# Optimization experiments

Hardware: AMD Instinct MI355X
Metric: run time of the kernel (lower is better)

## Reference

```python
import jax, jax.numpy as jnp
import numpy as np

N_NODES = 100000
N_EDGES = 3200000
IN_DIM = 256
HID = 16
OUT = 10


def setup_inputs() -> dict:
    key = jax.random.key(0)
    k1, k2, k3, k4, k5, k6 = jax.random.split(key, 6)
    x = jax.random.normal(k1, (N_NODES, IN_DIM), dtype=jnp.float32)
    edge_index = jax.random.randint(k2, (2, N_EDGES), 0, N_NODES, dtype=jnp.int64)
    # Glorot-style init for GCN weights, zeros for bias (PyG defaults)
    W1 = jax.random.normal(k3, (IN_DIM, HID), dtype=jnp.float32) * (1.0 / np.sqrt(IN_DIM))
    b1 = jnp.zeros((HID,), dtype=jnp.float32)
    W2 = jax.random.normal(k4, (HID, OUT), dtype=jnp.float32) * (1.0 / np.sqrt(HID))
    b2 = jnp.zeros((OUT,), dtype=jnp.float32)
    return {"x": x, "edge_index": edge_index, "W1": W1, "b1": b1, "W2": W2, "b2": b2}


def _gcn_conv(h, src, dst, W, b, num_nodes):
    # GCNConv(normalize=False): out_i = sum_{(j->i) in E} (h_j W) + b
    m = h @ W                                   # [N, F_out] small GEMM
    agg = jax.ops.segment_sum(m[src], dst, num_segments=num_nodes)  # gather+scatter-add
    return agg + b


def reference(x, edge_index, W1, b1, W2, b2):
    src = edge_index[0]  # message source (flow: source_to_target)
    dst = edge_index[1]
    n = x.shape[0]
    h = jax.nn.relu(_gcn_conv(x, src, dst, W1, b1, n))
    # F.dropout with module in eval mode -> identity
    out = _gcn_conv(h, src, dst, W2, b2, n)
    return out
```

## Files before the change

kernel.cpp:

```cpp
#include <hip/hip_runtime.h>
#include <hip/hip_bf16.h>
#include <stdint.h>

#define IN_DIM 256
#define HID 16
#define OUTD 10
#define BKT_SHIFT 8
#define BKT_W 256
#define PART_CH 4096
#define EPT 16

typedef short v8s __attribute__((ext_vector_type(8)));
typedef float v4f __attribute__((ext_vector_type(4)));

__device__ __forceinline__ float bf2f(unsigned short u) {
    return __uint_as_float(((unsigned int)u) << 16);
}
__device__ __forceinline__ unsigned short f2bf(float f) {
    unsigned int u = __float_as_uint(f);
    unsigned int lsb = (u >> 16) & 1u;
    u += 0x7fffu + lsb;
    return (unsigned short)(u >> 16);
}

__device__ __forceinline__ int load_dst(const void* ei, int n_edges, int e, int is64) {
    return is64 ? (int)((const long long*)ei)[(size_t)n_edges + e]
                : ((const int*)ei)[(size_t)n_edges + e];
}
__device__ __forceinline__ int load_src(const void* ei, int n_edges, int e, int is64) {
    return is64 ? (int)((const long long*)ei)[e] : ((const int*)ei)[e];
}

__global__ void setup_kernel(const void* __restrict__ x,
                             const void* __restrict__ W1,
                             const void* __restrict__ ei,
                             int n_nodes, int* __restrict__ flags,
                             int* __restrict__ bucket_cnt, int K) {
    int t = threadIdx.x;
    for (int i = t; i < K; i += blockDim.x) bucket_cnt[i] = 0;
    if (t < 64) {
        const unsigned short* xs = (const unsigned short*)x;
        const unsigned short* ws = (const unsigned short*)W1;
        bool badx = false, badw = false;
#pragma unroll
        for (int q = 0; q < 4; ++q) {
            float vx = bf2f(xs[t + 64 * q]);
            float vw = bf2f(ws[t + 64 * q]);
            if (!(vx > -1e4f && vx < 1e4f)) badx = true;
            if (!(vw > -1e4f && vw < 1e4f)) badw = true;
        }
        const unsigned long long* e64 = (const unsigned long long*)ei;
        bool big = false;
#pragma unroll
        for (int q = 0; q < 2; ++q)
            if (e64[t + 64 * q] >= (unsigned long long)n_nodes) big = true;
        int xf32 = __any(badx) ? 1 : 0;
        int wf32 = __any(badw) ? 1 : 0;
        int is64 = __any(big) ? 0 : 1;
        if (t == 0) { flags[0] = is64; flags[1] = xf32; flags[2] = wf32; }
    }
}

__global__ void w1prep_kernel(const void* __restrict__ W1p,
                              unsigned short* __restrict__ W1split,
                              const int* __restrict__ flags) {
    const int wf32 = flags[2];
    int i = threadIdx.x + blockIdx.x * blockDim.x;
    if (i >= IN_DIM * HID) return;
    float w = wf32 ? ((const float*)W1p)[i]
                   : bf2f(((const unsigned short*)W1p)[i]);
    unsigned short hi = f2bf(w);
    unsigned short lo = f2bf(w - bf2f(hi));
    int k = i >> 4, n = i & 15;
    int kk = k >> 5, qd = (k >> 3) & 3, j = k & 7;
    int idx = ((kk * 4 + qd) * 16 + n) * 8 + j;
    W1split[idx] = hi;
    W1split[4096 + idx] = lo;
}

__global__ void bhist_kernel(const void* __restrict__ ei, int n_edges,
                             int* __restrict__ bucket_cnt,
                             const int* __restrict__ flags, int K) {
    extern __shared__ int lh[];
    for (int i = threadIdx.x; i < K; i += blockDim.x) lh[i] = 0;
    __syncthreads();
    int is64 = flags[0];
    int t = blockIdx.x * blockDim.x + threadIdx.x;
    int stride = gridDim.x * blockDim.x;
    for (int e = t; e < n_edges; e += stride) {
        int d = load_dst(ei, n_edges, e, is64);
        atomicAdd(&lh[d >> BKT_SHIFT], 1);
    }
    __syncthreads();
    for (int i = threadIdx.x; i < K; i += blockDim.x)
        if (lh[i]) atomicAdd(&bucket_cnt[i], lh[i]);
}

__global__ void bscan_kernel(const int* __restrict__ bucket_cnt, int K,
                             int* __restrict__ bucket_off, int* __restrict__ bcur,
                             int* __restrict__ row_off, int n_nodes, int n_edges) {
    __shared__ int ts[256];
    int t = threadIdx.x;
    const int KP = (K + 255) / 256;
    int base = t * KP;
    int local[8];
    int s = 0;
    for (int q = 0; q < KP; ++q) {
        int idx = base + q;
        int v = (idx < K) ? bucket_cnt[idx] : 0;
        local[q] = v; s += v;
    }
    ts[t] = s;
    __syncthreads();
    for (int off = 1; off < 256; off <<= 1) {
        int v = (t >= off) ? ts[t - off] : 0;
        __syncthreads();
        ts[t] += v;
        __syncthreads();
    }
    int ex = ts[t] - s;
    for (int q = 0; q < KP; ++q) {
        int idx = base + q;
        if (idx < K) { bucket_off[idx] = ex; bcur[idx] = ex; }
        ex += local[q];
    }
    if (t == 255) bucket_off[K] = ex;
    if (t == 0) row_off[n_nodes] = n_edges;
}

__global__ void part_kernel(const void* __restrict__ ei, int n_edges,
                            int* __restrict__ bcur, unsigned int* __restrict__ pairs,
                            const int* __restrict__ flags, int K) {
    __shared__ int lh[512];
    __shared__ int gdelta[512];
    __shared__ int ts[256];
    __shared__ unsigned int spairs[PART_CH];
    __shared__ unsigned short sbkt[PART_CH];
    int begin = blockIdx.x * PART_CH;
    int is64 = flags[0];
    int t = threadIdx.x;
    lh[t] = 0; lh[t + 256] = 0;

    int dloc[EPT];
#pragma unroll
    for (int i = 0; i < EPT; ++i) {
        int e = begin + i * 256 + t;
        dloc[i] = (e < n_edges) ? load_dst(ei, n_edges, e, is64) : -1;
    }
    __syncthreads();
#pragma unroll
    for (int i = 0; i < EPT; ++i)
        if (dloc[i] >= 0) atomicAdd(&lh[dloc[i] >> BKT_SHIFT], 1);
    __syncthreads();

    int c0 = lh[2 * t], c1 = lh[2 * t + 1];
    int s = c0 + c1;
    ts[t] = s;
    __syncthreads();
    for (int off = 1; off < 256; off <<= 1) {
        int v = (t >= off) ? ts[t - off] : 0;
        __syncthreads();
        ts[t] += v;
        __syncthreads();
    }
    int ex = ts[t] - s;
    if (c0 > 0) gdelta[2 * t]     = atomicAdd(&bcur[2 * t], c0) - ex;
    if (c1 > 0) gdelta[2 * t + 1] = atomicAdd(&bcur[2 * t + 1], c1) - (ex + c0);
    __syncthreads();
    lh[2 * t] = ex; lh[2 * t + 1] = ex + c0;
    __syncthreads();

#pragma unroll
    for (int i = 0; i < EPT; ++i) {
        int e = begin + i * 256 + t;
        if (dloc[i] >= 0) {
            int srcv = load_src(ei, n_edges, e, is64);
            int b = dloc[i] >> BKT_SHIFT;
            int lpos = atomicAdd(&lh[b], 1);
            spairs[lpos] = ((unsigned)srcv << 8) | ((unsigned)dloc[i] & (BKT_W - 1));
            sbkt[lpos] = (unsigned short)b;
        }
    }
    __syncthreads();

    int total = n_edges - begin; if (total > PART_CH) total = PART_CH;
    for (int j = t; j < total; j += 256)
        pairs[gdelta[sbkt[j]] + j] = spairs[j];
}

__global__ void csr_kernel(const unsigned int* __restrict__ pairs,
                           const int* __restrict__ bucket_off,
                           int* __restrict__ row_off, int* __restrict__ csr_src,
                           int n_nodes) {
    __shared__ int deg[BKT_W];
    __shared__ int cur[BKT_W];
    __shared__ int ts[BKT_W];
    int blk = blockIdx.x;
    int nbase = blk << BKT_SHIFT;
    int NL = n_nodes - nbase; if (NL > BKT_W) NL = BKT_W;
    int beg = bucket_off[blk], end = bucket_off[blk + 1];
    int t = threadIdx.x;
    if (t < BKT_W) deg[t] = 0;
    __syncthreads();
    for (int k = beg + t; k < end; k += blockDim.x)
        atomicAdd(&deg[pairs[k] & (BKT_W - 1)], 1);
    __syncthreads();
    if (t < BKT_W) ts[t] = deg[t];
    __syncthreads();
    for (int off = 1; off < BKT_W; off <<= 1) {
        int v = 0;
        if (t < BKT_W && t >= off) v = ts[t - off];
        __syncthreads();
        if (t < BKT_W) ts[t] += v;
        __syncthreads();
    }
    if (t < BKT_W) {
        int ex = beg + ts[t] - deg[t];
        cur[t] = ex;
        if (t < NL) row_off[nbase + t] = ex;
    }
    __syncthreads();
    for (int k = beg + t; k < end; k += blockDim.x) {
        unsigned int p = pairs[k];
        int pos = atomicAdd(&cur[p & (BKT_W - 1)], 1);
        csr_src[pos] = (int)(p >> 8);
    }
}

__global__ __launch_bounds__(256, 4) void gemm1_kernel(
        const void* __restrict__ xp_,
        const unsigned short* __restrict__ W1split,
        unsigned short* __restrict__ m1, int n_nodes,
        const int* __restrict__ flags) {
    const int xf32 = flags[1];
    int t = threadIdx.x;
    int lane = t & 63;
    int wave = t >> 6;
    int col  = lane & 15;
    int quad = lane >> 4;
    int n_tiles = (n_nodes + 15) >> 4;
    const unsigned short* Whi = W1split;
    const unsigned short* Wlo = W1split + 4096;

    if (!xf32) {
        const unsigned short* x = (const unsigned short*)xp_;
        for (int tile = blockIdx.x * 4 + wave; tile < n_tiles; tile += gridDim.x * 4) {
            int row = tile * 16 + col;
            int r = row < n_nodes ? row : n_nodes - 1;
            const unsigned short* xp = x + (size_t)r * IN_DIM + quad * 8;
            v8s a[8];
#pragma unroll
            for (int kk = 0; kk < 8; ++kk)
                a[kk] = *(const v8s*)(xp + kk * 32);
            v4f acc1 = {0.f, 0.f, 0.f, 0.f};
            v4f acc2 = {0.f, 0.f, 0.f, 0.f};
#pragma unroll
            for (int kk = 0; kk < 8; ++kk) {
                v8s bh = *(const v8s*)&Whi[(kk * 64 + lane) * 8];
                v8s bl = *(const v8s*)&Wlo[(kk * 64 + lane) * 8];
                acc1 = __builtin_amdgcn_mfma_f32_16x16x32_bf16(a[kk], bh, acc1, 0, 0, 0);
                acc2 = __builtin_amdgcn_mfma_f32_16x16x32_bf16(a[kk], bl, acc2, 0, 0, 0);
            }
#pragma unroll
            for (int rg = 0; rg < 4; ++rg) {
                int node = tile * 16 + quad * 4 + rg;
                if (node < n_nodes)
                    m1[(size_t)node * HID + col] = f2bf(acc1[rg] + acc2[rg]);
            }
        }
    } else {
        const float* x = (const float*)xp_;
        for (int tile = blockIdx.x * 4 + wave; tile < n_tiles; tile += gridDim.x * 4) {
            int row = tile * 16 + col;
            int r = row < n_nodes ? row : n_nodes - 1;
            const float* xp = x + (size_t)r * IN_DIM + quad * 8;
            float4 u[16];
#pragma unroll
            for (int kk = 0; kk < 8; ++kk) {
                u[2 * kk]     = *(const float4*)(xp + kk * 32);
                u[2 * kk + 1] = *(const float4*)(xp + kk * 32 + 4);
            }
            v4f acc1 = {0.f, 0.f, 0.f, 0.f};
            v4f acc2 = {0.f, 0.f, 0.f, 0.f};
#pragma unroll
            for (int kk = 0; kk < 8; ++kk) {
                float uv[8] = {u[2 * kk].x,     u[2 * kk].y,
                               u[2 * kk].z,     u[2 * kk].w,
                               u[2 * kk + 1].x, u[2 * kk + 1].y,
                               u[2 * kk + 1].z, u[2 * kk + 1].w};
                v8s ahi, alo;
#pragma unroll
                for (int j = 0; j < 8; ++j) {
                    unsigned short hi = f2bf(uv[j]);
                    unsigned short lo = f2bf(uv[j] - bf2f(hi));
                    ahi[j] = (short)hi; alo[j] = (short)lo;
                }
                v8s bh = *(const v8s*)&Whi[(kk * 64 + lane) * 8];
                v8s bl = *(const v8s*)&Wlo[(kk * 64 + lane) * 8];
                acc1 = __builtin_amdgcn_mfma_f32_16x16x32_bf16(ahi, bh, acc1, 0, 0, 0);
                acc2 = __builtin_amdgcn_mfma_f32_16x16x32_bf16(ahi, bl, acc2, 0, 0, 0);
                acc2 = __builtin_amdgcn_mfma_f32_16x16x32_bf16(alo, bh, acc2, 0, 0, 0);
            }
#pragma unroll
            for (int rg = 0; rg < 4; ++rg) {
                int node = tile * 16 + quad * 4 + rg;
                if (node < n_nodes)
                    m1[(size_t)node * HID + col] = f2bf(acc1[rg] + acc2[rg]);
            }
        }
    }
}

__device__ __forceinline__ v4f gather_bf16(const unsigned short* __restrict__ src,
                                           const int* __restrict__ csr_src,
                                           int beg, int end, int q) {
    float a0 = 0.f, a1 = 0.f, a2 = 0.f, a3 = 0.f;
    int k = beg;
    for (; k + 16 <= end; k += 16) {
        uint2 v[16];
#pragma unroll
        for (int u = 0; u < 16; ++u) {
            int s = csr_src[k + u];
            v[u] = *(const uint2*)(src + (size_t)s * HID + q * 4);
        }
#pragma unroll
        for (int u = 0; u < 16; ++u) {
            a0 += bf2f((unsigned short)(v[u].x));
            a1 += bf2f((unsigned short)(v[u].x >> 16));
            a2 += bf2f((unsigned short)(v[u].y));
            a3 += bf2f((unsigned short)(v[u].y >> 16));
        }
    }
    for (; k + 4 <= end; k += 4) {
        uint2 v[4];
#pragma unroll
        for (int u = 0; u < 4; ++u) {
            int s = csr_src[k + u];
            v[u] = *(const uint2*)(src + (size_t)s * HID + q * 4);
        }
#pragma unroll
        for (int u = 0; u < 4; ++u) {
            a0 += bf2f((unsigned short)(v[u].x));
            a1 += bf2f((unsigned short)(v[u].x >> 16));
            a2 += bf2f((unsigned short)(v[u].y));
            a3 += bf2f((unsigned short)(v[u].y >> 16));
        }
    }
    for (; k < end; ++k) {
        int s = csr_src[k];
        uint2 v = *(const uint2*)(src + (size_t)s * HID + q * 4);
        a0 += bf2f((unsigned short)(v.x));
        a1 += bf2f((unsigned short)(v.x >> 16));
        a2 += bf2f((unsigned short)(v.y));
        a3 += bf2f((unsigned short)(v.y >> 16));
    }
    v4f r = {a0, a1, a2, a3};
    return r;
}

__global__ void agg1_kernel(const unsigned short* __restrict__ m1,
                            const int* __restrict__ row_off,
                            const int* __restrict__ csr_src,
                            const void* __restrict__ b1p,
                            unsigned short* __restrict__ h, int n_nodes,
                            const int* __restrict__ flags) {
    int t = blockIdx.x * blockDim.x + threadIdx.x;
    int node = t >> 2;
    if (node >= n_nodes) return;
    int q = t & 3;
    const int wf32 = flags[2];
    v4f a = gather_bf16(m1, csr_src, row_off[node], row_off[node + 1], q);
    float b0, b1v, b2v, b3;
    if (wf32) {
        const float* b = (const float*)b1p + q * 4;
        b0 = b[0]; b1v = b[1]; b2v = b[2]; b3 = b[3];
    } else {
        const unsigned short* b = (const unsigned short*)b1p + q * 4;
        b0 = bf2f(b[0]); b1v = bf2f(b[1]); b2v = bf2f(b[2]); b3 = bf2f(b[3]);
    }
    float r0 = fmaxf(a[0] + b0, 0.f);
    float r1 = fmaxf(a[1] + b1v, 0.f);
    float r2 = fmaxf(a[2] + b2v, 0.f);
    float r3 = fmaxf(a[3] + b3, 0.f);
    uint2 packed;
    packed.x = (unsigned int)f2bf(r0) | ((unsigned int)f2bf(r1) << 16);
    packed.y = (unsigned int)f2bf(r2) | ((unsigned int)f2bf(r3) << 16);
    *(uint2*)(h + (size_t)node * HID + q * 4) = packed;
}

__global__ void agg2_out_kernel(const unsigned short* __restrict__ h,
                                const int* __restrict__ row_off,
                                const int* __restrict__ csr_src,
                                const void* __restrict__ W2p,
                                const void* __restrict__ b2p,
                                void* __restrict__ out, int n_nodes,
                                const int* __restrict__ flags) {
    __shared__ float Ws[HID * OUTD];
    __shared__ float bs[OUTD];
    const int xf32 = flags[1], wf32 = flags[2];
    if (threadIdx.x < HID * OUTD)
        Ws[threadIdx.x] = wf32 ? ((const float*)W2p)[threadIdx.x]
                               : bf2f(((const unsigned short*)W2p)[threadIdx.x]);
    if (threadIdx.x < OUTD)
        bs[threadIdx.x] = wf32 ? ((const float*)b2p)[threadIdx.x]
                               : bf2f(((const unsigned short*)b2p)[threadIdx.x]);
    __syncthreads();

    int t = blockIdx.x * blockDim.x + threadIdx.x;
    int node = t >> 2;
    if (node >= n_nodes) return;
    int q = t & 3;
    v4f a = gather_bf16(h, csr_src, row_off[node], row_off[node + 1], q);

    float o[OUTD];
#pragma unroll
    for (int od = 0; od < OUTD; ++od) {
        float s = 0.f;
#pragma unroll
        for (int j = 0; j < 4; ++j)
            s = fmaf(a[j], Ws[(q * 4 + j) * OUTD + od], s);
        o[od] = s;
    }
#pragma unroll
    for (int od = 0; od < OUTD; ++od) {
        o[od] += __shfl_xor(o[od], 1);
        o[od] += __shfl_xor(o[od], 2);
        o[od] += bs[od];
    }

    if (xf32) {
        float2* po = (float2*)((float*)out + (size_t)node * OUTD);
        if (q == 0) {
            po[0] = make_float2(o[0], o[1]);
            po[1] = make_float2(o[2], o[3]);
        } else if (q == 1) {
            po[2] = make_float2(o[4], o[5]);
            po[3] = make_float2(o[6], o[7]);
        } else if (q == 2) {
            po[4] = make_float2(o[8], o[9]);
        }
    } else {
        unsigned int* po = (unsigned int*)((unsigned short*)out + (size_t)node * OUTD);
        if (q == 0) {
            po[0] = (unsigned int)f2bf(o[0]) | ((unsigned int)f2bf(o[1]) << 16);
            po[1] = (unsigned int)f2bf(o[2]) | ((unsigned int)f2bf(o[3]) << 16);
        } else if (q == 1) {
            po[2] = (unsigned int)f2bf(o[4]) | ((unsigned int)f2bf(o[5]) << 16);
            po[3] = (unsigned int)f2bf(o[6]) | ((unsigned int)f2bf(o[7]) << 16);
        } else if (q == 2) {
            po[4] = (unsigned int)f2bf(o[8]) | ((unsigned int)f2bf(o[9]) << 16);
        }
    }
}

__global__ void sentinel_kernel(float* __restrict__ out) {
    if (blockIdx.x == 0 && threadIdx.x < 16) out[threadIdx.x] = 123456.0f;
}

extern "C" void kernel_launch(void* const* d_in, const int* in_sizes, int n_in,
                              void* d_out, int out_size, void* d_ws, size_t ws_size,
                              hipStream_t stream) {
    const void* x  = d_in[0];
    const void* ei = d_in[1];
    const void* W1 = d_in[2];
    const void* b1 = d_in[3];
    const void* W2 = d_in[4];
    const void* b2 = d_in[5];

    const int n_nodes = in_sizes[0] / IN_DIM;
    const int n_edges = in_sizes[1] / 2;
    const int K = (n_nodes + BKT_W - 1) / BKT_W;

    char* p = (char*)d_ws;
    auto align = [](size_t v) { return (v + 255) & ~(size_t)255; };
    size_t off = 0;
    int* flags      = (int*)(p + off); off = align(off + 256);
    unsigned short* w1split = (unsigned short*)(p + off); off = align(off + 8192 * 2);
    int* bucket_cnt = (int*)(p + off); off = align(off + (size_t)K * 4);
    int* bucket_off = (int*)(p + off); off = align(off + ((size_t)K + 1) * 4);
    int* bcur       = (int*)(p + off); off = align(off + (size_t)K * 4);
    int* row_off    = (int*)(p + off); off = align(off + ((size_t)n_nodes + 1) * 4);
    int* csr_src    = (int*)(p + off); off = align(off + (size_t)n_edges * 4);
    size_t alias_base = off;
    unsigned int* pairs = (unsigned int*)(p + alias_base);
    unsigned short* m1 = (unsigned short*)(p + alias_base);
    unsigned short* h  = m1 + (size_t)n_nodes * HID;
    size_t alias_sz = (size_t)n_edges * 4;
    size_t mh_sz = (size_t)n_nodes * HID * 2 * 2;
    if (mh_sz > alias_sz) alias_sz = mh_sz;
    off = align(alias_base + alias_sz);

    if (ws_size < off) {
        sentinel_kernel<<<1, 64, 0, stream>>>((float*)d_out);
        return;
    }

    const size_t lds_k = (size_t)K * 4;

    setup_kernel<<<1, 256, 0, stream>>>(x, W1, ei, n_nodes, flags, bucket_cnt, K);
    w1prep_kernel<<<16, 256, 0, stream>>>(W1, w1split, flags);
    bhist_kernel<<<1024, 256, lds_k, stream>>>(ei, n_edges, bucket_cnt, flags, K);
    bscan_kernel<<<1, 256, 0, stream>>>(bucket_cnt, K, bucket_off, bcur,
                                        row_off, n_nodes, n_edges);
    part_kernel<<<(n_edges + PART_CH - 1) / PART_CH, 256, 0, stream>>>(
        ei, n_edges, bcur, pairs, flags, K);
    csr_kernel<<<K, 512, 0, stream>>>(pairs, bucket_off, row_off, csr_src, n_nodes);

    {
        int n_tiles16 = (n_nodes + 15) >> 4;
        int g1 = (n_tiles16 + 3) / 4;
        gemm1_kernel<<<g1, 256, 0, stream>>>(x, w1split, m1, n_nodes, flags);
    }

    {
        long long threads = (long long)n_nodes * 4;
        agg1_kernel<<<(int)((threads + 255) / 256), 256, 0, stream>>>(
            m1, row_off, csr_src, b1, h, n_nodes, flags);
    }

    {
        long long threads = (long long)n_nodes * 4;
        agg2_out_kernel<<<(int)((threads + 255) / 256), 256, 0, stream>>>(
            h, row_off, csr_src, W2, b2, d_out, n_nodes, flags);
    }
}
```

Before: 334.9 us.

## Replace bucketed CSR build with per-node degree counting and atomic scatter

Replaces the two-pass bucket partition and per-bucket CSR kernels with a per-node degree histogram built by global atomics, a hierarchical scan, and a direct atomic scatter into csr_src. The degree histogram runs inside the same launch as the first GEMM, in extra blocks, so the memory-bound edge read overlaps the dense x read. It also merges setup and W1 prep into one kernel, so fewer launches are needed. The cost is 3.2M global atomics on random node counters and a scatter with random write order, which makes the CSR neighbour order nondeterministic.

Result: slower. 643.4 us (+92.1%).

```diff
diff --git a/kernel.cpp b/kernel.cpp
--- a/kernel.cpp
+++ b/kernel.cpp
@@ -7,8 +7,6 @@
 #define OUTD 10
 #define BKT_SHIFT 8
 #define BKT_W 256
-#define PART_CH 4096
-#define EPT 16
 
 typedef short v8s __attribute__((ext_vector_type(8)));
 typedef float v4f __attribute__((ext_vector_type(4)));
@@ -31,44 +29,54 @@
     return is64 ? (int)((const long long*)ei)[e] : ((const int*)ei)[e];
 }
 
-__global__ void setup_kernel(const void* __restrict__ x,
-                             const void* __restrict__ W1,
-                             const void* __restrict__ ei,
-                             int n_nodes, int* __restrict__ flags,
-                             int* __restrict__ bucket_cnt, int K) {
-    int t = threadIdx.x;
-    for (int i = t; i < K; i += blockDim.x) bucket_cnt[i] = 0;
-    if (t < 64) {
-        const unsigned short* xs = (const unsigned short*)x;
-        const unsigned short* ws = (const unsigned short*)W1;
-        bool badx = false, badw = false;
-#pragma unroll
-        for (int q = 0; q < 4; ++q) {
-            float vx = bf2f(xs[t + 64 * q]);
-            float vw = bf2f(ws[t + 64 * q]);
-            if (!(vx > -1e4f && vx < 1e4f)) badx = true;
-            if (!(vw > -1e4f && vw < 1e4f)) badw = true;
-        }
-        const unsigned long long* e64 = (const unsigned long long*)ei;
-        bool big = false;
-#pragma unroll
-        for (int q = 0; q < 2; ++q)
-            if (e64[t + 64 * q] >= (unsigned long long)n_nodes) big = true;
-        int xf32 = __any(badx) ? 1 : 0;
-        int wf32 = __any(badw) ? 1 : 0;
-        int is64 = __any(big) ? 0 : 1;
-        if (t == 0) { flags[0] = is64; flags[1] = xf32; flags[2] = wf32; }
-    }
-}
-
-__global__ void w1prep_kernel(const void* __restrict__ W1p,
-                              unsigned short* __restrict__ W1split,
-                              const int* __restrict__ flags) {
-    const int wf32 = flags[2];
-    int i = threadIdx.x + blockIdx.x * blockDim.x;
-    if (i >= IN_DIM * HID) return;
-    float w = wf32 ? ((const float*)W1p)[i]
-                   : bf2f(((const unsigned short*)W1p)[i]);
+__global__ void setup_w1_kernel(const void* __restrict__ x,
+                                const void* __restrict__ W1,
+                                const void* __restrict__ ei,
+                                int n_nodes, int* __restrict__ flags,
+                                int* __restrict__ deg,
+                                unsigned short* __restrict__ W1split) {
+    int b = blockIdx.x, t = threadIdx.x;
+    int gid = b * blockDim.x + t;
+    for (int i = gid; i < n_nodes; i += gridDim.x * blockDim.x) deg[i] = 0;
+
+    if (b == 16) {
+        if (t < 64) {
+            const unsigned short* xs = (const unsigned short*)x;
+            const unsigned short* ws = (const unsigned short*)W1;
+            bool badx = false, badw = false;
+#pragma unroll
+            for (int q = 0; q < 4; ++q) {
+                float vx = bf2f(xs[t + 64 * q]);
+                float vw = bf2f(ws[t + 64 * q]);
+                if (!(vx > -1e4f && vx < 1e4f)) badx = true;
+                if (!(vw > -1e4f && vw < 1e4f)) badw = true;
+            }
+            const unsigned long long* e64 = (const unsigned long long*)ei;
+            bool big = false;
+#pragma unroll
+            for (int q = 0; q < 2; ++q)
+                if (e64[t + 64 * q] >= (unsigned long long)n_nodes) big = true;
+            int xf32 = __any(badx) ? 1 : 0;
+            int wf32 = __any(badw) ? 1 : 0;
+            int is64 = __any(big) ? 0 : 1;
+            if (t == 0) { flags[0] = is64; flags[1] = xf32; flags[2] = wf32; }
+        }
+        return;
+    }
+
+    __shared__ int swf32;
+    if (t == 0) swf32 = 0;
+    __syncthreads();
+    {
+        float vw = bf2f(((const unsigned short*)W1)[t]);
+        if (!(vw > -1e4f && vw < 1e4f)) swf32 = 1;
+    }
+    __syncthreads();
+    const int wf32 = swf32;
+
+    int i = b * 256 + t;
+    float w = wf32 ? ((const float*)W1)[i]
+                   : bf2f(((const unsigned short*)W1)[i]);
     unsigned short hi = f2bf(w);
     unsigned short lo = f2bf(w - bf2f(hi));
     int k = i >> 4, n = i & 15;
@@ -78,26 +86,119 @@
     W1split[4096 + idx] = lo;
 }
 
-__global__ void bhist_kernel(const void* __restrict__ ei, int n_edges,
-                             int* __restrict__ bucket_cnt,
-                             const int* __restrict__ flags, int K) {
-    extern __shared__ int lh[];
-    for (int i = threadIdx.x; i < K; i += blockDim.x) lh[i] = 0;
-    __syncthreads();
-    int is64 = flags[0];
-    int t = blockIdx.x * blockDim.x + threadIdx.x;
-    int stride = gridDim.x * blockDim.x;
-    for (int e = t; e < n_edges; e += stride) {
-        int d = load_dst(ei, n_edges, e, is64);
-        atomicAdd(&lh[d >> BKT_SHIFT], 1);
-    }
-    __syncthreads();
-    for (int i = threadIdx.x; i < K; i += blockDim.x)
-        if (lh[i]) atomicAdd(&bucket_cnt[i], lh[i]);
+__global__ __launch_bounds__(256, 4) void gemm1_hist_kernel(
+        const void* __restrict__ xp_,
+        const unsigned short* __restrict__ W1split,
+        unsigned short* __restrict__ m1,
+        const void* __restrict__ ei,
+        int* __restrict__ deg,
+        int n_nodes, int n_edges,
+        const int* __restrict__ flags, int g_gemm) {
+    int t = threadIdx.x;
+    if ((int)blockIdx.x >= g_gemm) {
+        int is64 = flags[0];
+        int vbid = blockIdx.x - g_gemm;
+        int stride = (gridDim.x - g_gemm) * 256;
+        for (int e = vbid * 256 + t; e < n_edges; e += stride) {
+            int d = load_dst(ei, n_edges, e, is64);
+            atomicAdd(&deg[d], 1);
+        }
+        return;
+    }
+    const int xf32 = flags[1];
+    int lane = t & 63;
+    int wave = t >> 6;
+    int col  = lane & 15;
+    int quad = lane >> 4;
+    int n_tiles = (n_nodes + 15) >> 4;
+    const unsigned short* Whi = W1split;
+    const unsigned short* Wlo = W1split + 4096;
+
+    if (!xf32) {
+        const unsigned short* x = (const unsigned short*)xp_;
+        for (int tile = blockIdx.x * 4 + wave; tile < n_tiles; tile += g_gemm * 4) {
+            int row = tile * 16 + col;
+            int r = row < n_nodes ? row : n_nodes - 1;
+            const unsigned short* xp = x + (size_t)r * IN_DIM + quad * 8;
+            v8s a[8];
+#pragma unroll
+            for (int kk = 0; kk < 8; ++kk)
+                a[kk] = *(const v8s*)(xp + kk * 32);
+            v4f acc1 = {0.f, 0.f, 0.f, 0.f};
+            v4f acc2 = {0.f, 0.f, 0.f, 0.f};
+#pragma unroll
+            for (int kk = 0; kk < 8; ++kk) {
+                v8s bh = *(const v8s*)&Whi[(kk * 64 + lane) * 8];
+                v8s bl = *(const v8s*)&Wlo[(kk * 64 + lane) * 8];
+                acc1 = __builtin_amdgcn_mfma_f32_16x16x32_bf16(a[kk], bh, acc1, 0, 0, 0);
+                acc2 = __builtin_amdgcn_mfma_f32_16x16x32_bf16(a[kk], bl, acc2, 0, 0, 0);
+            }
+#pragma unroll
+            for (int rg = 0; rg < 4; ++rg) {
+                int node = tile * 16 + quad * 4 + rg;
+                if (node < n_nodes)
+                    m1[(size_t)node * HID + col] = f2bf(acc1[rg] + acc2[rg]);
+            }
+        }
+    } else {
+        const float* x = (const float*)xp_;
+        for (int tile = blockIdx.x * 4 + wave; tile < n_tiles; tile += g_gemm * 4) {
+            int row = tile * 16 + col;
+            int r = row < n_nodes ? row : n_nodes - 1;
+            const float* xp = x + (size_t)r * IN_DIM + quad * 8;
+            float4 u[16];
+#pragma unroll
+            for (int kk = 0; kk < 8; ++kk) {
+                u[2 * kk]     = *(const float4*)(xp + kk * 32);
+                u[2 * kk + 1] = *(const float4*)(xp + kk * 32 + 4);
+            }
+            v4f acc1 = {0.f, 0.f, 0.f, 0.f};
+            v4f acc2 = {0.f, 0.f, 0.f, 0.f};
+#pragma unroll
+            for (int kk = 0; kk < 8; ++kk) {
+                float uv[8] = {u[2 * kk].x,     u[2 * kk].y,
+                               u[2 * kk].z,     u[2 * kk].w,
+                               u[2 * kk + 1].x, u[2 * kk + 1].y,
+                               u[2 * kk + 1].z, u[2 * kk + 1].w};
+                v8s ahi, alo;
+#pragma unroll
+                for (int j = 0; j < 8; ++j) {
+                    unsigned short hi = f2bf(uv[j]);
+                    unsigned short lo = f2bf(uv[j] - bf2f(hi));
+                    ahi[j] = (short)hi; alo[j] = (short)lo;
+                }
+                v8s bh = *(const v8s*)&Whi[(kk * 64 + lane) * 8];
+                v8s bl = *(const v8s*)&Wlo[(kk * 64 + lane) * 8];
+                acc1 = __builtin_amdgcn_mfma_f32_16x16x32_bf16(ahi, bh, acc1, 0, 0, 0);
+                acc2 = __builtin_amdgcn_mfma_f32_16x16x32_bf16(ahi, bl, acc2, 0, 0, 0);
+                acc2 = __builtin_amdgcn_mfma_f32_16x16x32_bf16(alo, bh, acc2, 0, 0, 0);
+            }
+#pragma unroll
+            for (int rg = 0; rg < 4; ++rg) {
+                int node = tile * 16 + quad * 4 + rg;
+                if (node < n_nodes)
+                    m1[(size_t)node * HID + col] = f2bf(acc1[rg] + acc2[rg]);
+            }
+        }
+    }
+}
+
+__global__ void scanA_kernel(const int* __restrict__ deg, int n_nodes,
+                             int* __restrict__ bucket_cnt) {
+    __shared__ int red[256];
+    int b = blockIdx.x, t = threadIdx.x;
+    int n = b * 256 + t;
+    red[t] = (n < n_nodes) ? deg[n] : 0;
+    __syncthreads();
+    for (int o = 128; o > 0; o >>= 1) {
+        if (t < o) red[t] += red[t + o];
+        __syncthreads();
+    }
+    if (t == 0) bucket_cnt[b] = red[0];
 }
 
 __global__ void bscan_kernel(const int* __restrict__ bucket_cnt, int K,
-                             int* __restrict__ bucket_off, int* __restrict__ bcur,
+                             int* __restrict__ bucket_off,
                              int* __restrict__ row_off, int n_nodes, int n_edges) {
     __shared__ int ts[256];
     int t = threadIdx.x;
@@ -121,41 +222,22 @@
     int ex = ts[t] - s;
     for (int q = 0; q < KP; ++q) {
         int idx = base + q;
-        if (idx < K) { bucket_off[idx] = ex; bcur[idx] = ex; }
+        if (idx < K) bucket_off[idx] = ex;
         ex += local[q];
     }
     if (t == 255) bucket_off[K] = ex;
     if (t == 0) row_off[n_nodes] = n_edges;
 }
 
-__global__ void part_kernel(const void* __restrict__ ei, int n_edges,
-                            int* __restrict__ bcur, unsigned int* __restrict__ pairs,
-                            const int* __restrict__ flags, int K) {
-    __shared__ int lh[512];
-    __shared__ int gdelta[512];
+__global__ void scanC_kernel(const int* __restrict__ deg,
+                             const int* __restrict__ bucket_off,
+                             int* __restrict__ row_off, int* __restrict__ cur,
+                             int n_nodes) {
     __shared__ int ts[256];
-    __shared__ unsigned int spairs[PART_CH];
-    __shared__ unsigned short sbkt[PART_CH];
-    int begin = blockIdx.x * PART_CH;
-    int is64 = flags[0];
-    int t = threadIdx.x;
-    lh[t] = 0; lh[t + 256] = 0;
-
-    int dloc[EPT];
-#pragma unroll
-    for (int i = 0; i < EPT; ++i) {
-        int e = begin + i * 256 + t;
-        dloc[i] = (e < n_edges) ? load_dst(ei, n_edges, e, is64) : -1;
-    }
-    __syncthreads();
-#pragma unroll
-    for (int i = 0; i < EPT; ++i)
-        if (dloc[i] >= 0) atomicAdd(&lh[dloc[i] >> BKT_SHIFT], 1);
-    __syncthreads();
-
-    int c0 = lh[2 * t], c1 = lh[2 * t + 1];
-    int s = c0 + c1;
-    ts[t] = s;
+    int b = blockIdx.x, t = threadIdx.x;
+    int n = b * 256 + t;
+    int d = (n < n_nodes) ? deg[n] : 0;
+    ts[t] = d;
     __syncthreads();
     for (int off = 1; off < 256; off <<= 1) {
         int v = (t >= off) ? ts[t - off] : 0;
@@ -163,150 +245,29 @@
         ts[t] += v;
         __syncthreads();
     }
-    int ex = ts[t] - s;
-    if (c0 > 0) gdelta[2 * t]     = atomicAdd(&bcur[2 * t], c0) - ex;
-    if (c1 > 0) gdelta[2 * t + 1] = atomicAdd(&bcur[2 * t + 1], c1) - (ex + c0);
-    __syncthreads();
-    lh[2 * t] = ex; lh[2 * t + 1] = ex + c0;
-    __syncthreads();
-
-#pragma unroll
-    for (int i = 0; i < EPT; ++i) {
-        int e = begin + i * 256 + t;
-        if (dloc[i] >= 0) {
-            int srcv = load_src(ei, n_edges, e, is64);
-            int b = dloc[i] >> BKT_SHIFT;
-            int lpos = atomicAdd(&lh[b], 1);
-            spairs[lpos] = ((unsigned)srcv << 8) | ((unsigned)dloc[i] & (BKT_W - 1));
-            sbkt[lpos] = (unsigned short)b;
-        }
-    }
-    __syncthreads();
-
-    int total = n_edges - begin; if (total > PART_CH) total = PART_CH;
-    for (int j = t; j < total; j += 256)
-        pairs[gdelta[sbkt[j]] + j] = spairs[j];
-}
-
-__global__ void csr_kernel(const unsigned int* __restrict__ pairs,
-                           const int* __restrict__ bucket_off,
-                           int* __restrict__ row_off, int* __restrict__ csr_src,
-                           int n_nodes) {
-    __shared__ int deg[BKT_W];
-    __shared__ int cur[BKT_W];
-    __shared__ int ts[BKT_W];
-    int blk = blockIdx.x;
-    int nbase = blk << BKT_SHIFT;
-    int NL = n_nodes - nbase; if (NL > BKT_W) NL = BKT_W;
-    int beg = bucket_off[blk], end = bucket_off[blk + 1];
+    int ex = bucket_off[b] + ts[t] - d;
+    if (n < n_nodes) { row_off[n] = ex; cur[n] = ex; }
+}
+
+__global__ __launch_bounds__(256) void scatter_kernel(
+        const void* __restrict__ ei, int n_edges,
+        int* __restrict__ cur, int* __restrict__ csr_src,
+        const int* __restrict__ flags) {
+    int is64 = flags[0];
+    int base = blockIdx.x * 1024;
     int t = threadIdx.x;
-    if (t < BKT_W) deg[t] = 0;
-    __syncthreads();
-    for (int k = beg + t; k < end; k += blockDim.x)
-        atomicAdd(&deg[pairs[k] & (BKT_W - 1)], 1);
-    __syncthreads();
-    if (t < BKT_W) ts[t] = deg[t];
-    __syncthreads();
-    for (int off = 1; off < BKT_W; off <<= 1) {
-        int v = 0;
-        if (t < BKT_W && t >= off) v = ts[t - off];
-        __syncthreads();
-        if (t < BKT_W) ts[t] += v;
-        __syncthreads();
-    }
-    if (t < BKT_W) {
-        int ex = beg + ts[t] - deg[t];
-        cur[t] = ex;
-        if (t < NL) row_off[nbase + t] = ex;
-    }
-    __syncthreads();
-    for (int k = beg + t; k < end; k += blockDim.x) {
-        unsigned int p = pairs[k];
-        int pos = atomicAdd(&cur[p & (BKT_W - 1)], 1);
-        csr_src[pos] = (int)(p >> 8);
-    }
-}
-
-__global__ __launch_bounds__(256, 4) void gemm1_kernel(
-        const void* __restrict__ xp_,
-        const unsigned short* __restrict__ W1split,
-        unsigned short* __restrict__ m1, int n_nodes,
-        const int* __restrict__ flags) {
-    const int xf32 = flags[1];
-    int t = threadIdx.x;
-    int lane = t & 63;
-    int wave = t >> 6;
-    int col  = lane & 15;
-    int quad = lane >> 4;
-    int n_tiles = (n_nodes + 15) >> 4;
-    const unsigned short* Whi = W1split;
-    const unsigned short* Wlo = W1split + 4096;
-
-    if (!xf32) {
-        const unsigned short* x = (const unsigned short*)xp_;
-        for (int tile = blockIdx.x * 4 + wave; tile < n_tiles; tile += gridDim.x * 4) {
-            int row = tile * 16 + col;
-            int r = row < n_nodes ? row : n_nodes - 1;
-            const unsigned short* xp = x + (size_t)r * IN_DIM + quad * 8;
-            v8s a[8];
-#pragma unroll
-            for (int kk = 0; kk < 8; ++kk)
-                a[kk] = *(const v8s*)(xp + kk * 32);
-            v4f acc1 = {0.f, 0.f, 0.f, 0.f};
-            v4f acc2 = {0.f, 0.f, 0.f, 0.f};
-#pragma unroll
-            for (int kk = 0; kk < 8; ++kk) {
-                v8s bh = *(const v8s*)&Whi[(kk * 64 + lane) * 8];
-                v8s bl = *(const v8s*)&Wlo[(kk * 64 + lane) * 8];
-                acc1 = __builtin_amdgcn_mfma_f32_16x16x32_bf16(a[kk], bh, acc1, 0, 0, 0);
-                acc2 = __builtin_amdgcn_mfma_f32_16x16x32_bf16(a[kk], bl, acc2, 0, 0, 0);
-            }
-#pragma unroll
-            for (int rg = 0; rg < 4; ++rg) {
-                int node = tile * 16 + quad * 4 + rg;
-                if (node < n_nodes)
-                    m1[(size_t)node * HID + col] = f2bf(acc1[rg] + acc2[rg]);
-            }
-        }
-    } else {
-        const float* x = (const float*)xp_;
-        for (int tile = blockIdx.x * 4 + wave; tile < n_tiles; tile += gridDim.x * 4) {
-            int row = tile * 16 + col;
-            int r = row < n_nodes ? row : n_nodes - 1;
-            const float* xp = x + (size_t)r * IN_DIM + quad * 8;
-            float4 u[16];
-#pragma unroll
-            for (int kk = 0; kk < 8; ++kk) {
-                u[2 * kk]     = *(const float4*)(xp + kk * 32);
-                u[2 * kk + 1] = *(const float4*)(xp + kk * 32 + 4);
-            }
-            v4f acc1 = {0.f, 0.f, 0.f, 0.f};
-            v4f acc2 = {0.f, 0.f, 0.f, 0.f};
-#pragma unroll
-            for (int kk = 0; kk < 8; ++kk) {
-                float uv[8] = {u[2 * kk].x,     u[2 * kk].y,
-                               u[2 * kk].z,     u[2 * kk].w,
-                               u[2 * kk + 1].x, u[2 * kk + 1].y,
-                               u[2 * kk + 1].z, u[2 * kk + 1].w};
-                v8s ahi, alo;
-#pragma unroll
-                for (int j = 0; j < 8; ++j) {
-                    unsigned short hi = f2bf(uv[j]);
-                    unsigned short lo = f2bf(uv[j] - bf2f(hi));
-                    ahi[j] = (short)hi; alo[j] = (short)lo;
-                }
-                v8s bh = *(const v8s*)&Whi[(kk * 64 + lane) * 8];
-                v8s bl = *(const v8s*)&Wlo[(kk * 64 + lane) * 8];
-                acc1 = __builtin_amdgcn_mfma_f32_16x16x32_bf16(ahi, bh, acc1, 0, 0, 0);
-                acc2 = __builtin_amdgcn_mfma_f32_16x16x32_bf16(ahi, bl, acc2, 0, 0, 0);
-                acc2 = __builtin_amdgcn_mfma_f32_16x16x32_bf16(alo, bh, acc2, 0, 0, 0);
-            }
-#pragma unroll
-            for (int rg = 0; rg < 4; ++rg) {
-                int node = tile * 16 + quad * 4 + rg;
-                if (node < n_nodes)
-                    m1[(size_t)node * HID + col] = f2bf(acc1[rg] + acc2[rg]);
-            }
+    int d[4], s[4];
+#pragma unroll
+    for (int r = 0; r < 4; ++r) {
+        int e = base + r * 256 + t;
+        d[r] = (e < n_edges) ? load_dst(ei, n_edges, e, is64) : -1;
+        s[r] = (e < n_edges) ? load_src(ei, n_edges, e, is64) : 0;
+    }
+#pragma unroll
+    for (int r = 0; r < 4; ++r) {
+        if (d[r] >= 0) {
+            int pos = atomicAdd(&cur[d[r]], 1);
+            csr_src[pos] = s[r];
         }
     }
 }
@@ -476,41 +437,36 @@
     size_t off = 0;
     int* flags      = (int*)(p + off); off = align(off + 256);
     unsigned short* w1split = (unsigned short*)(p + off); off = align(off + 8192 * 2);
+    int* deg        = (int*)(p + off); off = align(off + (size_t)n_nodes * 4);
+    int* cur        = (int*)(p + off); off = align(off + (size_t)n_nodes * 4);
     int* bucket_cnt = (int*)(p + off); off = align(off + (size_t)K * 4);
     int* bucket_off = (int*)(p + off); off = align(off + ((size_t)K + 1) * 4);
-    int* bcur       = (int*)(p + off); off = align(off + (size_t)K * 4);
     int* row_off    = (int*)(p + off); off = align(off + ((size_t)n_nodes + 1) * 4);
     int* csr_src    = (int*)(p + off); off = align(off + (size_t)n_edges * 4);
-    size_t alias_base = off;
-    unsigned int* pairs = (unsigned int*)(p + alias_base);
-    unsigned short* m1 = (unsigned short*)(p + alias_base);
-    unsigned short* h  = m1 + (size_t)n_nodes * HID;
-    size_t alias_sz = (size_t)n_edges * 4;
-    size_t mh_sz = (size_t)n_nodes * HID * 2 * 2;
-    if (mh_sz > alias_sz) alias_sz = mh_sz;
-    off = align(alias_base + alias_sz);
+    unsigned short* m1 = (unsigned short*)(p + off); off = align(off + (size_t)n_nodes * HID * 2);
+    unsigned short* h  = (unsigned short*)(p + off); off = align(off + (size_t)n_nodes * HID * 2);
 
     if (ws_size < off) {
         sentinel_kernel<<<1, 64, 0, stream>>>((float*)d_out);
         return;
     }
 
-    const size_t lds_k = (size_t)K * 4;
-
-    setup_kernel<<<1, 256, 0, stream>>>(x, W1, ei, n_nodes, flags, bucket_cnt, K);
-    w1prep_kernel<<<16, 256, 0, stream>>>(W1, w1split, flags);
-    bhist_kernel<<<1024, 256, lds_k, stream>>>(ei, n_edges, bucket_cnt, flags, K);
-    bscan_kernel<<<1, 256, 0, stream>>>(bucket_cnt, K, bucket_off, bcur,
+    const int n_tiles16 = (n_nodes + 15) >> 4;
+    const int g_gemm = (n_tiles16 + 3) / 4;
+    const int g_hist = 1024;
+
+    setup_w1_kernel<<<17, 256, 0, stream>>>(x, W1, ei, n_nodes, flags, deg, w1split);
+
+    gemm1_hist_kernel<<<g_gemm + g_hist, 256, 0, stream>>>(
+        x, w1split, m1, ei, deg, n_nodes, n_edges, flags, g_gemm);
+
+    scanA_kernel<<<K, 256, 0, stream>>>(deg, n_nodes, bucket_cnt);
+    bscan_kernel<<<1, 256, 0, stream>>>(bucket_cnt, K, bucket_off,
                                         row_off, n_nodes, n_edges);
-    part_kernel<<<(n_edges + PART_CH - 1) / PART_CH, 256, 0, stream>>>(
-        ei, n_edges, bcur, pairs, flags, K);
-    csr_kernel<<<K, 512, 0, stream>>>(pairs, bucket_off, row_off, csr_src, n_nodes);
-
-    {
-        int n_tiles16 = (n_nodes + 15) >> 4;
-        int g1 = (n_tiles16 + 3) / 4;
-        gemm1_kernel<<<g1, 256, 0, stream>>>(x, w1split, m1, n_nodes, flags);
-    }
+    scanC_kernel<<<K, 256, 0, stream>>>(deg, bucket_off, row_off, cur, n_nodes);
+
+    scatter_kernel<<<(n_edges + 1023) / 1024, 256, 0, stream>>>(
+        ei, n_edges, cur, csr_src, flags);
 
     {
         long long threads = (long long)n_nodes * 4;
```

## Fuse setup with W1 prep and co-schedule GEMM1 with destination histogram

Applied to the files above, without the earlier changes.

Merges the setup and W1-split kernels into one launch: 16 blocks split the weights and one block writes the dtype flags. The dense GEMM1 and the destination-bucket histogram now run as disjoint block ranges of one launch, so the compute-bound GEMM overlaps the memory-bound edge scan. Because m1 must now exist alongside pairs, the workspace no longer aliases them, and the histogram uses a fixed 512-entry LDS array. Partition chunk and edges-per-thread are halved for more blocks. Risks: W1split blocks recompute the dtype flag locally, the LDS histogram silently assumes K<=512, and the workspace grows.

After: 348.9 us. +4.2%, slower.

```diff
diff --git a/kernel.cpp b/kernel.cpp
--- a/kernel.cpp
+++ b/kernel.cpp
@@ -7,8 +7,8 @@
 #define OUTD 10
 #define BKT_SHIFT 8
 #define BKT_W 256
-#define PART_CH 4096
-#define EPT 16
+#define PART_CH 2048
+#define EPT 8
 
 typedef short v8s __attribute__((ext_vector_type(8)));
 typedef float v4f __attribute__((ext_vector_type(4)));
@@ -31,44 +31,54 @@
     return is64 ? (int)((const long long*)ei)[e] : ((const int*)ei)[e];
 }
 
-__global__ void setup_kernel(const void* __restrict__ x,
-                             const void* __restrict__ W1,
-                             const void* __restrict__ ei,
-                             int n_nodes, int* __restrict__ flags,
-                             int* __restrict__ bucket_cnt, int K) {
-    int t = threadIdx.x;
-    for (int i = t; i < K; i += blockDim.x) bucket_cnt[i] = 0;
-    if (t < 64) {
-        const unsigned short* xs = (const unsigned short*)x;
-        const unsigned short* ws = (const unsigned short*)W1;
-        bool badx = false, badw = false;
-#pragma unroll
-        for (int q = 0; q < 4; ++q) {
-            float vx = bf2f(xs[t + 64 * q]);
-            float vw = bf2f(ws[t + 64 * q]);
-            if (!(vx > -1e4f && vx < 1e4f)) badx = true;
-            if (!(vw > -1e4f && vw < 1e4f)) badw = true;
-        }
-        const unsigned long long* e64 = (const unsigned long long*)ei;
-        bool big = false;
-#pragma unroll
-        for (int q = 0; q < 2; ++q)
-            if (e64[t + 64 * q] >= (unsigned long long)n_nodes) big = true;
-        int xf32 = __any(badx) ? 1 : 0;
-        int wf32 = __any(badw) ? 1 : 0;
-        int is64 = __any(big) ? 0 : 1;
-        if (t == 0) { flags[0] = is64; flags[1] = xf32; flags[2] = wf32; }
-    }
-}
-
-__global__ void w1prep_kernel(const void* __restrict__ W1p,
-                              unsigned short* __restrict__ W1split,
-                              const int* __restrict__ flags) {
-    const int wf32 = flags[2];
-    int i = threadIdx.x + blockIdx.x * blockDim.x;
-    if (i >= IN_DIM * HID) return;
-    float w = wf32 ? ((const float*)W1p)[i]
-                   : bf2f(((const unsigned short*)W1p)[i]);
+__global__ void setup_w1_kernel(const void* __restrict__ x,
+                                const void* __restrict__ W1,
+                                const void* __restrict__ ei,
+                                int n_nodes, int* __restrict__ flags,
+                                int* __restrict__ bucket_cnt, int K,
+                                unsigned short* __restrict__ W1split) {
+    int b = blockIdx.x, t = threadIdx.x;
+    int gid = b * blockDim.x + t;
+    for (int i = gid; i < K; i += gridDim.x * blockDim.x) bucket_cnt[i] = 0;
+
+    if (b == 16) {
+        if (t < 64) {
+            const unsigned short* xs = (const unsigned short*)x;
+            const unsigned short* ws = (const unsigned short*)W1;
+            bool badx = false, badw = false;
+#pragma unroll
+            for (int q = 0; q < 4; ++q) {
+                float vx = bf2f(xs[t + 64 * q]);
+                float vw = bf2f(ws[t + 64 * q]);
+                if (!(vx > -1e4f && vx < 1e4f)) badx = true;
+                if (!(vw > -1e4f && vw < 1e4f)) badw = true;
+            }
+            const unsigned long long* e64 = (const unsigned long long*)ei;
+            bool big = false;
+#pragma unroll
+            for (int q = 0; q < 2; ++q)
+                if (e64[t + 64 * q] >= (unsigned long long)n_nodes) big = true;
+            int xf32 = __any(badx) ? 1 : 0;
+            int wf32 = __any(badw) ? 1 : 0;
+            int is64 = __any(big) ? 0 : 1;
+            if (t == 0) { flags[0] = is64; flags[1] = xf32; flags[2] = wf32; }
+        }
+        return;
+    }
+
+    __shared__ int swf32;
+    if (t == 0) swf32 = 0;
+    __syncthreads();
+    {
+        float vw = bf2f(((const unsigned short*)W1)[t]);
+        if (!(vw > -1e4f && vw < 1e4f)) swf32 = 1;
+    }
+    __syncthreads();
+    const int wf32 = swf32;
+
+    int i = b * 256 + t;
+    float w = wf32 ? ((const float*)W1)[i]
+                   : bf2f(((const unsigned short*)W1)[i]);
     unsigned short hi = f2bf(w);
     unsigned short lo = f2bf(w - bf2f(hi));
     int k = i >> 4, n = i & 15;
@@ -78,22 +88,107 @@
     W1split[4096 + idx] = lo;
 }
 
-__global__ void bhist_kernel(const void* __restrict__ ei, int n_edges,
-                             int* __restrict__ bucket_cnt,
-                             const int* __restrict__ flags, int K) {
-    extern __shared__ int lh[];
-    for (int i = threadIdx.x; i < K; i += blockDim.x) lh[i] = 0;
-    __syncthreads();
-    int is64 = flags[0];
-    int t = blockIdx.x * blockDim.x + threadIdx.x;
-    int stride = gridDim.x * blockDim.x;
-    for (int e = t; e < n_edges; e += stride) {
-        int d = load_dst(ei, n_edges, e, is64);
-        atomicAdd(&lh[d >> BKT_SHIFT], 1);
-    }
-    __syncthreads();
-    for (int i = threadIdx.x; i < K; i += blockDim.x)
-        if (lh[i]) atomicAdd(&bucket_cnt[i], lh[i]);
+__global__ __launch_bounds__(256, 4) void gemm1_bhist_kernel(
+        const void* __restrict__ xp_,
+        const unsigned short* __restrict__ W1split,
+        unsigned short* __restrict__ m1,
+        const void* __restrict__ ei,
+        int* __restrict__ bucket_cnt,
+        int n_nodes, int n_edges, int K,
+        const int* __restrict__ flags, int g_gemm) {
+    __shared__ int lh[512];
+    int t = threadIdx.x;
+    if ((int)blockIdx.x >= g_gemm) {
+        for (int i = t; i < 512; i += 256) lh[i] = 0;
+        __syncthreads();
+        int is64 = flags[0];
+        int vbid = blockIdx.x - g_gemm;
+        int stride = (gridDim.x - g_gemm) * 256;
+        for (int e = vbid * 256 + t; e < n_edges; e += stride) {
+            int d = load_dst(ei, n_edges, e, is64);
+            atomicAdd(&lh[d >> BKT_SHIFT], 1);
+        }
+        __syncthreads();
+        for (int i = t; i < K; i += 256)
+            if (lh[i]) atomicAdd(&bucket_cnt[i], lh[i]);
+        return;
+    }
+    const int xf32 = flags[1];
+    int lane = t & 63;
+    int wave = t >> 6;
+    int col  = lane & 15;
+    int quad = lane >> 4;
+    int n_tiles = (n_nodes + 15) >> 4;
+    const unsigned short* Whi = W1split;
+    const unsigned short* Wlo = W1split + 4096;
+
+    if (!xf32) {
+        const unsigned short* x = (const unsigned short*)xp_;
+        for (int tile = blockIdx.x * 4 + wave; tile < n_tiles; tile += g_gemm * 4) {
+            int row = tile * 16 + col;
+            int r = row < n_nodes ? row : n_nodes - 1;
+            const unsigned short* xp = x + (size_t)r * IN_DIM + quad * 8;
+            v8s a[8];
+#pragma unroll
+            for (int kk = 0; kk < 8; ++kk)
+                a[kk] = *(const v8s*)(xp + kk * 32);
+            v4f acc1 = {0.f, 0.f, 0.f, 0.f};
+            v4f acc2 = {0.f, 0.f, 0.f, 0.f};
+#pragma unroll
+            for (int kk = 0; kk < 8; ++kk) {
+                v8s bh = *(const v8s*)&Whi[(kk * 64 + lane) * 8];
+                v8s bl = *(const v8s*)&Wlo[(kk * 64 + lane) * 8];
+                acc1 = __builtin_amdgcn_mfma_f32_16x16x32_bf16(a[kk], bh, acc1, 0, 0, 0);
+                acc2 = __builtin_amdgcn_mfma_f32_16x16x32_bf16(a[kk], bl, acc2, 0, 0, 0);
+            }
+#pragma unroll
+            for (int rg = 0; rg < 4; ++rg) {
+                int node = tile * 16 + quad * 4 + rg;
+                if (node < n_nodes)
+                    m1[(size_t)node * HID + col] = f2bf(acc1[rg] + acc2[rg]);
+            }
+        }
+    } else {
+        const float* x = (const float*)xp_;
+        for (int tile = blockIdx.x * 4 + wave; tile < n_tiles; tile += g_gemm * 4) {
+            int row = tile * 16 + col;
+            int r = row < n_nodes ? row : n_nodes - 1;
+            const float* xp = x + (size_t)r * IN_DIM + quad * 8;
+            float4 u[16];
+#pragma unroll
+            for (int kk = 0; kk < 8; ++kk) {
+                u[2 * kk]     = *(const float4*)(xp + kk * 32);
+                u[2 * kk + 1] = *(const float4*)(xp + kk * 32 + 4);
+            }
+            v4f acc1 = {0.f, 0.f, 0.f, 0.f};
+            v4f acc2 = {0.f, 0.f, 0.f, 0.f};
+#pragma unroll
+            for (int kk = 0; kk < 8; ++kk) {
+                float uv[8] = {u[2 * kk].x,     u[2 * kk].y,
+                               u[2 * kk].z,     u[2 * kk].w,
+                               u[2 * kk + 1].x, u[2 * kk + 1].y,
+                               u[2 * kk + 1].z, u[2 * kk + 1].w};
+                v8s ahi, alo;
+#pragma unroll
+                for (int j = 0; j < 8; ++j) {
+                    unsigned short hi = f2bf(uv[j]);
+                    unsigned short lo = f2bf(uv[j] - bf2f(hi));
+                    ahi[j] = (short)hi; alo[j] = (short)lo;
+                }
+                v8s bh = *(const v8s*)&Whi[(kk * 64 + lane) * 8];
+                v8s bl = *(const v8s*)&Wlo[(kk * 64 + lane) * 8];
+                acc1 = __builtin_amdgcn_mfma_f32_16x16x32_bf16(ahi, bh, acc1, 0, 0, 0);
+                acc2 = __builtin_amdgcn_mfma_f32_16x16x32_bf16(ahi, bl, acc2, 0, 0, 0);
+                acc2 = __builtin_amdgcn_mfma_f32_16x16x32_bf16(alo, bh, acc2, 0, 0, 0);
+            }
+#pragma unroll
+            for (int rg = 0; rg < 4; ++rg) {
+                int node = tile * 16 + quad * 4 + rg;
+                if (node < n_nodes)
+                    m1[(size_t)node * HID + col] = f2bf(acc1[rg] + acc2[rg]);
+            }
+        }
+    }
 }
 
 __global__ void bscan_kernel(const int* __restrict__ bucket_cnt, int K,
@@ -224,90 +319,6 @@
         unsigned int p = pairs[k];
         int pos = atomicAdd(&cur[p & (BKT_W - 1)], 1);
         csr_src[pos] = (int)(p >> 8);
-    }
-}
-
-__global__ __launch_bounds__(256, 4) void gemm1_kernel(
-        const void* __restrict__ xp_,
-        const unsigned short* __restrict__ W1split,
-        unsigned short* __restrict__ m1, int n_nodes,
-        const int* __restrict__ flags) {
-    const int xf32 = flags[1];
-    int t = threadIdx.x;
-    int lane = t & 63;
-    int wave = t >> 6;
-    int col  = lane & 15;
-    int quad = lane >> 4;
-    int n_tiles = (n_nodes + 15) >> 4;
-    const unsigned short* Whi = W1split;
-    const unsigned short* Wlo = W1split + 4096;
-
-    if (!xf32) {
-        const unsigned short* x = (const unsigned short*)xp_;
-        for (int tile = blockIdx.x * 4 + wave; tile < n_tiles; tile += gridDim.x * 4) {
-            int row = tile * 16 + col;
-            int r = row < n_nodes ? row : n_nodes - 1;
-            const unsigned short* xp = x + (size_t)r * IN_DIM + quad * 8;
-            v8s a[8];
-#pragma unroll
-            for (int kk = 0; kk < 8; ++kk)
-                a[kk] = *(const v8s*)(xp + kk * 32);
-            v4f acc1 = {0.f, 0.f, 0.f, 0.f};
-            v4f acc2 = {0.f, 0.f, 0.f, 0.f};
-#pragma unroll
-            for (int kk = 0; kk < 8; ++kk) {
-                v8s bh = *(const v8s*)&Whi[(kk * 64 + lane) * 8];
-                v8s bl = *(const v8s*)&Wlo[(kk * 64 + lane) * 8];
-                acc1 = __builtin_amdgcn_mfma_f32_16x16x32_bf16(a[kk], bh, acc1, 0, 0, 0);
-                acc2 = __builtin_amdgcn_mfma_f32_16x16x32_bf16(a[kk], bl, acc2, 0, 0, 0);
-            }
-#pragma unroll
-            for (int rg = 0; rg < 4; ++rg) {
-                int node = tile * 16 + quad * 4 + rg;
-                if (node < n_nodes)
-                    m1[(size_t)node * HID + col] = f2bf(acc1[rg] + acc2[rg]);
-            }
-        }
-    } else {
-        const float* x = (const float*)xp_;
-        for (int tile = blockIdx.x * 4 + wave; tile < n_tiles; tile += gridDim.x * 4) {
-            int row = tile * 16 + col;
-            int r = row < n_nodes ? row : n_nodes - 1;
-            const float* xp = x + (size_t)r * IN_DIM + quad * 8;
-            float4 u[16];
-#pragma unroll
-            for (int kk = 0; kk < 8; ++kk) {
-                u[2 * kk]     = *(const float4*)(xp + kk * 32);
-                u[2 * kk + 1] = *(const float4*)(xp + kk * 32 + 4);
-            }
-            v4f acc1 = {0.f, 0.f, 0.f, 0.f};
-            v4f acc2 = {0.f, 0.f, 0.f, 0.f};
-#pragma unroll
-            for (int kk = 0; kk < 8; ++kk) {
-                float uv[8] = {u[2 * kk].x,     u[2 * kk].y,
-                               u[2 * kk].z,     u[2 * kk].w,
-                               u[2 * kk + 1].x, u[2 * kk + 1].y,
-                               u[2 * kk + 1].z, u[2 * kk + 1].w};
-                v8s ahi, alo;
-#pragma unroll
-                for (int j = 0; j < 8; ++j) {
-                    unsigned short hi = f2bf(uv[j]);
-                    unsigned short lo = f2bf(uv[j] - bf2f(hi));
-                    ahi[j] = (short)hi; alo[j] = (short)lo;
-                }
-                v8s bh = *(const v8s*)&Whi[(kk * 64 + lane) * 8];
-                v8s bl = *(const v8s*)&Wlo[(kk * 64 + lane) * 8];
-                acc1 = __builtin_amdgcn_mfma_f32_16x16x32_bf16(ahi, bh, acc1, 0, 0, 0);
-                acc2 = __builtin_amdgcn_mfma_f32_16x16x32_bf16(ahi, bl, acc2, 0, 0, 0);
-                acc2 = __builtin_amdgcn_mfma_f32_16x16x32_bf16(alo, bh, acc2, 0, 0, 0);
-            }
-#pragma unroll
-            for (int rg = 0; rg < 4; ++rg) {
-                int node = tile * 16 + quad * 4 + rg;
-                if (node < n_nodes)
-                    m1[(size_t)node * HID + col] = f2bf(acc1[rg] + acc2[rg]);
-            }
-        }
     }
 }
 
@@ -481,36 +492,32 @@
     int* bcur       = (int*)(p + off); off = align(off + (size_t)K * 4);
     int* row_off    = (int*)(p + off); off = align(off + ((size_t)n_nodes + 1) * 4);
     int* csr_src    = (int*)(p + off); off = align(off + (size_t)n_edges * 4);
-    size_t alias_base = off;
-    unsigned int* pairs = (unsigned int*)(p + alias_base);
-    unsigned short* m1 = (unsigned short*)(p + alias_base);
-    unsigned short* h  = m1 + (size_t)n_nodes * HID;
-    size_t alias_sz = (size_t)n_edges * 4;
-    size_t mh_sz = (size_t)n_nodes * HID * 2 * 2;
-    if (mh_sz > alias_sz) alias_sz = mh_sz;
-    off = align(alias_base + alias_sz);
+    unsigned int* pairs = (unsigned int*)(p + off); off = align(off + (size_t)n_edges * 4);
+    unsigned short* m1 = (unsigned short*)(p + off); off = align(off + (size_t)n_nodes * HID * 2);
+    unsigned short* h  = (unsigned short*)(p + off); off = align(off + (size_t)n_nodes * HID * 2);
 
     if (ws_size < off) {
         sentinel_kernel<<<1, 64, 0, stream>>>((float*)d_out);
         return;
     }
 
-    const size_t lds_k = (size_t)K * 4;
-
-    setup_kernel<<<1, 256, 0, stream>>>(x, W1, ei, n_nodes, flags, bucket_cnt, K);
-    w1prep_kernel<<<16, 256, 0, stream>>>(W1, w1split, flags);
-    bhist_kernel<<<1024, 256, lds_k, stream>>>(ei, n_edges, bucket_cnt, flags, K);
+    const int n_tiles16 = (n_nodes + 15) >> 4;
+    const int g_gemm = (n_tiles16 + 3) / 4;
+    const int g_hist = 512;
+
+    setup_w1_kernel<<<17, 256, 0, stream>>>(x, W1, ei, n_nodes, flags,
+                                            bucket_cnt, K, w1split);
+
+    gemm1_bhist_kernel<<<g_gemm + g_hist, 256, 0, stream>>>(
+        x, w1split, m1, ei, bucket_cnt, n_nodes, n_edges, K, flags, g_gemm);
+
     bscan_kernel<<<1, 256, 0, stream>>>(bucket_cnt, K, bucket_off, bcur,
                                         row_off, n_nodes, n_edges);
+
     part_kernel<<<(n_edges + PART_CH - 1) / PART_CH, 256, 0, stream>>>(
         ei, n_edges, bcur, pairs, flags, K);
+
     csr_kernel<<<K, 512, 0, stream>>>(pairs, bucket_off, row_off, csr_src, n_nodes);
-
-    {
-        int n_tiles16 = (n_nodes + 15) >> 4;
-        int g1 = (n_tiles16 + 3) / 4;
-        gemm1_kernel<<<g1, 256, 0, stream>>>(x, w1split, m1, n_nodes, flags);
-    }
 
     {
         long long threads = (long long)n_nodes * 4;
```
